# Performance work log

Hardware: AMD Instinct MI355X
Metric: run time of the kernel (lower is better)

The kernel has to match this reference:

```python
import jax, jax.numpy as jnp
import numpy as np


def _binarize(w):
    # BinaryConnect-style deterministic binarization: sign with 0 -> +1.
    # Straight-through estimator: identity gradient.
    b = jnp.where(w >= 0, 1.0, -1.0).astype(w.dtype)
    return w + jax.lax.stop_gradient(b - w)


def setup_inputs() -> dict:
    key = jax.random.key(0)
    ks = jax.random.split(key, 9)
    B = 65536
    x = jax.random.normal(ks[0], (B, 784), dtype=jnp.float32)
    # Kaiming-ish latent fp32 weights for the binary layers, fp32 final layer.
    w1 = jax.random.normal(ks[1], (512, 784), dtype=jnp.float32) * (1.0 / np.sqrt(784))
    b1 = jnp.zeros((512,), dtype=jnp.float32)
    w2 = jax.random.normal(ks[2], (512, 512), dtype=jnp.float32) * (1.0 / np.sqrt(512))
    b2 = jnp.zeros((512,), dtype=jnp.float32)
    w3 = jax.random.normal(ks[3], (512, 512), dtype=jnp.float32) * (1.0 / np.sqrt(512))
    b3 = jnp.zeros((512,), dtype=jnp.float32)
    w4 = jax.random.normal(ks[4], (10, 512), dtype=jnp.float32) * (1.0 / np.sqrt(512))
    b4 = jnp.zeros((10,), dtype=jnp.float32)
    return {"x": x, "w1": w1, "b1": b1, "w2": w2, "b2": b2,
            "w3": w3, "b3": b3, "w4": w4, "b4": b4}


def reference(x, w1, b1, w2, b2, w3, b3, w4, b4):
    # fc1..fc3: binarized-weight linear + ReLU; fc4: plain fp32 linear.
    h = jax.nn.relu(x @ _binarize(w1).T + b1)
    h = jax.nn.relu(h @ _binarize(w2).T + b2)
    h = jax.nn.relu(h @ _binarize(w3).T + b3)
    return h @ w4.T + b4
```

## Files before the change

kernel.cpp:

```cpp
#include <hip/hip_runtime.h>
#include <hip/hip_bf16.h>
#include <stdint.h>


typedef __attribute__((ext_vector_type(8))) short short8;
typedef __attribute__((ext_vector_type(4))) float f32x4;

#define THREADS 512
#define BM      64
#define HID     512
#define K1      784
#define K1P     832
#define BK      32
#define NK1     (K1P / BK)
#define NK2     (HID / BK)

#define M1_OFF  0
#define M1_BYTES (8 * NK1 * 256)
#define M2_OFF  (M1_OFF + M1_BYTES)
#define M2_BYTES (8 * NK2 * 256)
#define M3_OFF  (M2_OFF + M2_BYTES)
#define W4_OFF  (M3_OFF + M2_BYTES)
#define W4_BYTES (16 * HID * 2)
#define WS_BYTES (W4_OFF + W4_BYTES)

#define H_BYTES  (BM * HID * 2)
#define XBUF0    H_BYTES
#define XTILE_SZ (BM * BK * 2)
#define LUT_OFF  (XBUF0 + 2 * XTILE_SZ)
#define LDS_TOTAL (LUT_OFF + 128)

#define LGKM0_BARRIER()  do {                                   \
    asm volatile("s_waitcnt lgkmcnt(0)" ::: "memory");          \
    __builtin_amdgcn_s_barrier();                               \
} while (0)

__device__ __forceinline__ unsigned short bfu(float f) {
    __hip_bfloat16 h = __float2bfloat16(f);
    return *reinterpret_cast<unsigned short*>(&h);
}

__device__ __forceinline__ unsigned cvtpk(float lo, float hi) {
    unsigned d;
    asm("v_cvt_pk_bf16_f32 %0, %1, %2" : "=v"(d) : "v"(lo), "v"(hi));
    return d;
}

__global__ void prep_weights(const float* __restrict__ w1, const float* __restrict__ w2,
                             const float* __restrict__ w3, const float* __restrict__ w4,
                             unsigned char* __restrict__ ws)
{
    int id = blockIdx.x * blockDim.x + threadIdx.x;
    const int T1 = 8 * NK1 * 64;
    const int T2 = 8 * NK2 * 64;
    const int T4 = 16 * (HID / 16);

    if (id < T1) {
        int wn = id / (NK1 * 64), rem = id % (NK1 * 64);
        int kt = rem / 64, lane = rem % 64;
        int lr = lane & 15, lg = lane >> 4;
        unsigned m = 0;
#pragma unroll
        for (int nf = 0; nf < 4; ++nf) {
            int n = wn * 64 + nf * 16 + lr;
#pragma unroll
            for (int j = 0; j < 8; ++j) {
                int k = kt * BK + lg * 8 + j;
                if (k < K1 && w1[n * K1 + k] < 0.0f) m |= 1u << (nf * 8 + j);
            }
        }
        *(unsigned*)(ws + M1_OFF + (size_t)id * 4) = m;
        return;
    }
    id -= T1;
    if (id < 2 * T2) {
        const float* w = (id < T2) ? w2 : w3;
        unsigned base = (id < T2) ? M2_OFF : M3_OFF;
        int iid = (id < T2) ? id : id - T2;
        int wn = iid / (NK2 * 64), rem = iid % (NK2 * 64);
        int kt = rem / 64, lane = rem % 64;
        int lr = lane & 15, lg = lane >> 4;
        unsigned m = 0;
#pragma unroll
        for (int nf = 0; nf < 4; ++nf) {
            int n = wn * 64 + nf * 16 + lr;
#pragma unroll
            for (int j = 0; j < 8; ++j) {
                int k = kt * BK + lg * 8 + j;
                if (w[n * HID + k] < 0.0f) m |= 1u << (nf * 8 + j);
            }
        }
        *(unsigned*)(ws + base + (size_t)iid * 4) = m;
        return;
    }
    id -= 2 * T2;
    if (id < T4) {
        int n = id / (HID / 16), j = id % (HID / 16);
        int kp0 = j * 16;
        unsigned short v[16];
#pragma unroll
        for (int i = 0; i < 16; ++i)
            v[i] = (n < 10) ? bfu(w4[n * HID + kp0 + i]) : 0;
        unsigned off = W4_OFF + n * 1024 + kp0 * 2;
        *(short8*)(ws + off)      = *(short8*)&v[0];
        *(short8*)(ws + off + 16) = *(short8*)&v[8];
    }
}

__global__ __launch_bounds__(THREADS, 4)
void fused_mlp(const float* __restrict__ x,
               const unsigned char* __restrict__ ws,
               const float* __restrict__ b1, const float* __restrict__ b2,
               const float* __restrict__ b3, const float* __restrict__ b4,
               float* __restrict__ out)
{
    extern __shared__ unsigned char lds[];
    const int tid  = threadIdx.x;
    const int lane = tid & 63;
    const int wave = tid >> 6;
    const int lr   = lane & 15;
    const int lg   = lane >> 4;
    const int row_base = blockIdx.x * BM;
    const unsigned swz = (unsigned)((lr & 7) << 4);

    if (tid < 16) {
        unsigned e0 = ((tid & 1) ? 0xBF80u : 0x3F80u)
                    | (((tid & 2) ? 0xBF80u : 0x3F80u) << 16);
        unsigned e1 = ((tid & 4) ? 0xBF80u : 0x3F80u)
                    | (((tid & 8) ? 0xBF80u : 0x3F80u) << 16);
        uint2 e; e.x = e0; e.y = e1;
        *(uint2*)(lds + LUT_OFF + tid * 8) = e;
    }

    f32x4 acc[4][4];
    auto zeroAcc = [&]() {
#pragma unroll
        for (int nf = 0; nf < 4; ++nf)
#pragma unroll
            for (int mg = 0; mg < 4; ++mg)
                acc[nf][mg] = (f32x4){0.f, 0.f, 0.f, 0.f};
    };

    auto h_off = [&](int row, int bc) -> unsigned {
        return ((unsigned)(row * 1024 + bc)) ^ (unsigned)((row & 7) << 4);
    };

    auto epilogueToH = [&](const float* __restrict__ bias) {
#pragma unroll
        for (int nf = 0; nf < 4; ++nf) {
            const int n0 = wave * 64 + nf * 16 + lg * 4;
            float4 bv = *(const float4*)(bias + n0);
#pragma unroll
            for (int mg = 0; mg < 4; ++mg) {
                float v0 = acc[nf][mg][0] + bv.x; v0 = v0 > 0.f ? v0 : 0.f;
                float v1 = acc[nf][mg][1] + bv.y; v1 = v1 > 0.f ? v1 : 0.f;
                float v2 = acc[nf][mg][2] + bv.z; v2 = v2 > 0.f ? v2 : 0.f;
                float v3 = acc[nf][mg][3] + bv.w; v3 = v3 > 0.f ? v3 : 0.f;
                uint2 d; d.x = cvtpk(v0, v1); d.y = cvtpk(v2, v3);
                int row = mg * 16 + lr;
                unsigned off = ((unsigned)(row * 1024 + n0 * 2)) ^ (unsigned)((row & 7) << 4);
                *(uint2*)(lds + off) = d;
            }
        }
    };

    auto lutA = [&](unsigned m, int nf) -> short8 {
        unsigned lo = (m >> (nf * 8)) & 15u;
        unsigned hi = (m >> (nf * 8 + 4)) & 15u;
        union { short8 s; uint2 d[2]; } r;
        r.d[0] = *(const uint2*)(lds + LUT_OFF + lo * 8);
        r.d[1] = *(const uint2*)(lds + LUT_OFF + hi * 8);
        return r.s;
    };

    {
        zeroAcc();
        const unsigned char* mb1 = ws + M1_OFF + wave * (NK1 * 256) + lane * 4;
        const int srow = tid >> 3, sq = tid & 7;
        const float* xrow = x + (size_t)(row_base + srow) * K1;
        const unsigned s_off = (((unsigned)(srow * 64 + sq * 8)) ^ (unsigned)((srow & 7) << 4)) + XBUF0;
        const unsigned xbase = (((unsigned)(lr * 64 + lg * 16)) ^ swz) + XBUF0;

        auto xload = [&](int t) -> float4 {
            int col = t * BK + sq * 4;
            return (col < K1) ? *(const float4*)(xrow + col)
                              : make_float4(0.f, 0.f, 0.f, 0.f);
        };
        auto stage_write = [&](int buf, float4 v) {
            uint2 pk; pk.x = cvtpk(v.x, v.y); pk.y = cvtpk(v.z, v.w);
            *(uint2*)(lds + s_off + buf * XTILE_SZ) = pk;
        };
        auto mload1 = [&](int t) -> unsigned {
            int tc = t < NK1 ? t : NK1 - 1;
            return *(const unsigned*)(mb1 + tc * 256);
        };
        auto l1_compute = [&](int buf, unsigned m) {
            unsigned xb = xbase + buf * XTILE_SZ;
            short8 B0 = *(const short8*)(lds + xb);
            short8 B1 = *(const short8*)(lds + xb + 1024);
            short8 B2 = *(const short8*)(lds + xb + 2048);
            short8 B3 = *(const short8*)(lds + xb + 3072);
            __builtin_amdgcn_s_setprio(1);
#pragma unroll
            for (int nf = 0; nf < 4; ++nf) {
                short8 A = lutA(m, nf);
                acc[nf][0] = __builtin_amdgcn_mfma_f32_16x16x32_bf16(A, B0, acc[nf][0], 0, 0, 0);
                acc[nf][1] = __builtin_amdgcn_mfma_f32_16x16x32_bf16(A, B1, acc[nf][1], 0, 0, 0);
                acc[nf][2] = __builtin_amdgcn_mfma_f32_16x16x32_bf16(A, B2, acc[nf][2], 0, 0, 0);
                acc[nf][3] = __builtin_amdgcn_mfma_f32_16x16x32_bf16(A, B3, acc[nf][3], 0, 0, 0);
            }
            __builtin_amdgcn_s_setprio(0);
        };

        stage_write(0, xload(0));
        float4 xc = xload(1), xn = xload(2);
        unsigned mc = mload1(0), mn = mload1(1);
        LGKM0_BARRIER();

#pragma unroll 1
        for (int kt = 0; kt < NK1; ++kt) {
            float4 xnew = xload(kt + 3);
            unsigned mnew = mload1(kt + 2);
            l1_compute(kt & 1, mc);
            stage_write((kt + 1) & 1, xc);
            xc = xn; xn = xnew; mc = mn; mn = mnew;
            LGKM0_BARRIER();
        }

        epilogueToH(b1);
        LGKM0_BARRIER();
    }

#pragma unroll 1
    for (int layer = 0; layer < 2; ++layer) {
        const unsigned char* mb = ws + (layer == 0 ? M2_OFF : M3_OFF)
                                + wave * (NK2 * 256) + lane * 4;
        const float* bias = (layer == 0) ? b2 : b3;

        zeroAcc();

        auto mload2 = [&](int t) -> unsigned {
            int tc = t < NK2 ? t : NK2 - 1;
            return *(const unsigned*)(mb + tc * 256);
        };
        auto l23_compute = [&](int kt, unsigned m) {
            unsigned hb = (((unsigned)(lr * 1024 + kt * 64 + lg * 16)) ^ swz);
            short8 B0 = *(const short8*)(lds + hb);
            short8 B1 = *(const short8*)(lds + hb + 16384);
            short8 B2 = *(const short8*)(lds + hb + 32768);
            short8 B3 = *(const short8*)(lds + hb + 49152);
            __builtin_amdgcn_s_setprio(1);
#pragma unroll
            for (int nf = 0; nf < 4; ++nf) {
                short8 A = lutA(m, nf);
                acc[nf][0] = __builtin_amdgcn_mfma_f32_16x16x32_bf16(A, B0, acc[nf][0], 0, 0, 0);
                acc[nf][1] = __builtin_amdgcn_mfma_f32_16x16x32_bf16(A, B1, acc[nf][1], 0, 0, 0);
                acc[nf][2] = __builtin_amdgcn_mfma_f32_16x16x32_bf16(A, B2, acc[nf][2], 0, 0, 0);
                acc[nf][3] = __builtin_amdgcn_mfma_f32_16x16x32_bf16(A, B3, acc[nf][3], 0, 0, 0);
            }
            __builtin_amdgcn_s_setprio(0);
        };

        unsigned q0 = mload2(0), q1 = mload2(1), q2 = mload2(2), q3 = mload2(3);
#pragma unroll 1
        for (int kt = 0; kt < NK2; kt += 4) {
            l23_compute(kt + 0, q0); q0 = mload2(kt + 4);
            l23_compute(kt + 1, q1); q1 = mload2(kt + 5);
            l23_compute(kt + 2, q2); q2 = mload2(kt + 6);
            l23_compute(kt + 3, q3); q3 = mload2(kt + 7);
        }

        LGKM0_BARRIER();
        epilogueToH(bias);
        LGKM0_BARRIER();
    }

    if (wave < 4) {
        const unsigned char* w4b = ws + W4_OFF + lr * 1024 + lg * 16;
        const int m = wave * 16 + lr;
        short8 w4f[16];
#pragma unroll
        for (int kt = 0; kt < NK2; ++kt)
            w4f[kt] = *(const short8*)(w4b + kt * 64);
        f32x4 acc4 = (f32x4){0.f, 0.f, 0.f, 0.f};
#pragma unroll
        for (int kt = 0; kt < NK2; ++kt) {
            short8 a = *(const short8*)(lds + h_off(m, kt * 64 + lg * 16));
            acc4 = __builtin_amdgcn_mfma_f32_16x16x32_bf16(a, w4f[kt], acc4, 0, 0, 0);
        }
        if (lr < 10) {
            float bv = b4[lr];
#pragma unroll
            for (int r = 0; r < 4; ++r) {
                int row = row_base + wave * 16 + lg * 4 + r;
                out[(size_t)row * 10 + lr] = acc4[r] + bv;
            }
        }
    }
}

extern "C" void kernel_launch(void* const* d_in, const int* in_sizes, int n_in,
                              void* d_out, int out_size, void* d_ws, size_t ws_size,
                              hipStream_t stream) {
    const float* x  = (const float*)d_in[0];
    const float* w1 = (const float*)d_in[1];
    const float* b1 = (const float*)d_in[2];
    const float* w2 = (const float*)d_in[3];
    const float* b2 = (const float*)d_in[4];
    const float* w3 = (const float*)d_in[5];
    const float* b3 = (const float*)d_in[6];
    const float* w4 = (const float*)d_in[7];
    const float* b4 = (const float*)d_in[8];
    float* out = (float*)d_out;
    unsigned char* ws = (unsigned char*)d_ws;

    if (ws_size < (size_t)WS_BYTES) return;

    const int B = in_sizes[0] / K1;
    const int nblk = B / BM;

    (void)hipFuncSetAttribute((const void*)fused_mlp,
                              hipFuncAttributeMaxDynamicSharedMemorySize, LDS_TOTAL);

    const int prep_total = 8 * NK1 * 64 + 2 * (8 * NK2 * 64) + 16 * (HID / 16);
    prep_weights<<<(prep_total + 255) / 256, 256, 0, stream>>>(w1, w2, w3, w4, ws);
    fused_mlp<<<nblk, THREADS, LDS_TOTAL, stream>>>(x, ws, b1, b2, b3, b4, out);
}
```

Measured before the change: 106.8 us.

## Switch binary-MLP GEMMs from 16x16x32 to 32x32x16 bf16 MFMA tiles

Replaces the 16 per-step 16x16x32 MFMAs with 8 32x32x16 MFMAs on four 32x32 accumulator tiles. The weight sign-mask packing and the activation LDS fragment addressing are rewritten to match the 32-lane operand layout. The sign LUT is replicated four times in LDS and indexed by lane&3 to spread bank accesses. The aim is fewer MFMA issues and fewer operand loads per K step, at the cost of a new fragment layout and a rewritten epilogue that must stay correct.

```diff
diff --git a/kernel.cpp b/kernel.cpp
--- a/kernel.cpp
+++ b/kernel.cpp
@@ -3,8 +3,9 @@
 #include <stdint.h>
 
 
-typedef __attribute__((ext_vector_type(8))) short short8;
-typedef __attribute__((ext_vector_type(4))) float f32x4;
+typedef __attribute__((ext_vector_type(8)))  short short8;
+typedef __attribute__((ext_vector_type(4)))  float f32x4;
+typedef __attribute__((ext_vector_type(16))) float f32x16;
 
 #define THREADS 512
 #define BM      64
@@ -28,7 +29,7 @@
 #define XBUF0    H_BYTES
 #define XTILE_SZ (BM * BK * 2)
 #define LUT_OFF  (XBUF0 + 2 * XTILE_SZ)
-#define LDS_TOTAL (LUT_OFF + 128)
+#define LDS_TOTAL (LUT_OFF + 512)
 
 #define LGKM0_BARRIER()  do {                                   \
     asm volatile("s_waitcnt lgkmcnt(0)" ::: "memory");          \
@@ -58,15 +59,16 @@
     if (id < T1) {
         int wn = id / (NK1 * 64), rem = id % (NK1 * 64);
         int kt = rem / 64, lane = rem % 64;
-        int lr = lane & 15, lg = lane >> 4;
+        int r32 = lane & 31, g32 = lane >> 5;
         unsigned m = 0;
 #pragma unroll
-        for (int nf = 0; nf < 4; ++nf) {
-            int n = wn * 64 + nf * 16 + lr;
+        for (int f = 0; f < 4; ++f) {
+            int n = wn * 64 + (f >> 1) * 32 + r32;
+            int kb = kt * BK + (f & 1) * 16 + g32 * 8;
 #pragma unroll
             for (int j = 0; j < 8; ++j) {
-                int k = kt * BK + lg * 8 + j;
-                if (k < K1 && w1[n * K1 + k] < 0.0f) m |= 1u << (nf * 8 + j);
+                int k = kb + j;
+                if (k < K1 && w1[n * K1 + k] < 0.0f) m |= 1u << (f * 8 + j);
             }
         }
         *(unsigned*)(ws + M1_OFF + (size_t)id * 4) = m;
@@ -79,16 +81,15 @@
         int iid = (id < T2) ? id : id - T2;
         int wn = iid / (NK2 * 64), rem = iid % (NK2 * 64);
         int kt = rem / 64, lane = rem % 64;
-        int lr = lane & 15, lg = lane >> 4;
+        int r32 = lane & 31, g32 = lane >> 5;
         unsigned m = 0;
 #pragma unroll
-        for (int nf = 0; nf < 4; ++nf) {
-            int n = wn * 64 + nf * 16 + lr;
-#pragma unroll
-            for (int j = 0; j < 8; ++j) {
-                int k = kt * BK + lg * 8 + j;
-                if (w[n * HID + k] < 0.0f) m |= 1u << (nf * 8 + j);
-            }
+        for (int f = 0; f < 4; ++f) {
+            int n = wn * 64 + (f >> 1) * 32 + r32;
+            int kb = kt * BK + (f & 1) * 16 + g32 * 8;
+#pragma unroll
+            for (int j = 0; j < 8; ++j)
+                if (w[n * HID + kb + j] < 0.0f) m |= 1u << (f * 8 + j);
         }
         *(unsigned*)(ws + base + (size_t)iid * 4) = m;
         return;
@@ -120,58 +121,64 @@
     const int wave = tid >> 6;
     const int lr   = lane & 15;
     const int lg   = lane >> 4;
+    const int l31  = lane & 31;
+    const int l5   = lane >> 5;
     const int row_base = blockIdx.x * BM;
-    const unsigned swz = (unsigned)((lr & 7) << 4);
-
-    if (tid < 16) {
-        unsigned e0 = ((tid & 1) ? 0xBF80u : 0x3F80u)
-                    | (((tid & 2) ? 0xBF80u : 0x3F80u) << 16);
-        unsigned e1 = ((tid & 4) ? 0xBF80u : 0x3F80u)
-                    | (((tid & 8) ? 0xBF80u : 0x3F80u) << 16);
+    const unsigned swz = (unsigned)((lane & 7) << 4);
+    const unsigned lutbase = LUT_OFF + (unsigned)((lane & 3) << 7);
+
+    if (tid < 64) {
+        int entry = tid & 15;
+        unsigned e0 = ((entry & 1) ? 0xBF80u : 0x3F80u)
+                    | (((entry & 2) ? 0xBF80u : 0x3F80u) << 16);
+        unsigned e1 = ((entry & 4) ? 0xBF80u : 0x3F80u)
+                    | (((entry & 8) ? 0xBF80u : 0x3F80u) << 16);
         uint2 e; e.x = e0; e.y = e1;
-        *(uint2*)(lds + LUT_OFF + tid * 8) = e;
-    }
-
-    f32x4 acc[4][4];
+        *(uint2*)(lds + LUT_OFF + (tid >> 4) * 128 + entry * 8) = e;
+    }
+
+    f32x16 acc00, acc01, acc10, acc11;
     auto zeroAcc = [&]() {
-#pragma unroll
-        for (int nf = 0; nf < 4; ++nf)
-#pragma unroll
-            for (int mg = 0; mg < 4; ++mg)
-                acc[nf][mg] = (f32x4){0.f, 0.f, 0.f, 0.f};
+        f32x16 z;
+#pragma unroll
+        for (int i = 0; i < 16; ++i) z[i] = 0.f;
+        acc00 = z; acc01 = z; acc10 = z; acc11 = z;
     };
 
     auto h_off = [&](int row, int bc) -> unsigned {
         return ((unsigned)(row * 1024 + bc)) ^ (unsigned)((row & 7) << 4);
     };
 
+    auto lutA = [&](unsigned m, int f) -> short8 {
+        unsigned lo = (m >> (f * 8)) & 15u;
+        unsigned hi = (m >> (f * 8 + 4)) & 15u;
+        union { short8 s; uint2 d[2]; } r;
+        r.d[0] = *(const uint2*)(lds + lutbase + lo * 8);
+        r.d[1] = *(const uint2*)(lds + lutbase + hi * 8);
+        return r.s;
+    };
+
+    auto epi = [&](const f32x16& a, int nt, int bt, const float* __restrict__ bias) {
+        const int brow = bt * 32 + l31;
+#pragma unroll
+        for (int q = 0; q < 4; ++q) {
+            int n0 = wave * 64 + nt * 32 + 8 * q + 4 * l5;
+            float4 bv = *(const float4*)(bias + n0);
+            float v0 = a[4 * q + 0] + bv.x; v0 = v0 > 0.f ? v0 : 0.f;
+            float v1 = a[4 * q + 1] + bv.y; v1 = v1 > 0.f ? v1 : 0.f;
+            float v2 = a[4 * q + 2] + bv.z; v2 = v2 > 0.f ? v2 : 0.f;
+            float v3 = a[4 * q + 3] + bv.w; v3 = v3 > 0.f ? v3 : 0.f;
+            uint2 d; d.x = cvtpk(v0, v1); d.y = cvtpk(v2, v3);
+            unsigned off = ((unsigned)(brow * 1024 + n0 * 2)) ^ (unsigned)((brow & 7) << 4);
+            *(uint2*)(lds + off) = d;
+        }
+    };
     auto epilogueToH = [&](const float* __restrict__ bias) {
-#pragma unroll
-        for (int nf = 0; nf < 4; ++nf) {
-            const int n0 = wave * 64 + nf * 16 + lg * 4;
-            float4 bv = *(const float4*)(bias + n0);
-#pragma unroll
-            for (int mg = 0; mg < 4; ++mg) {
-                float v0 = acc[nf][mg][0] + bv.x; v0 = v0 > 0.f ? v0 : 0.f;
-                float v1 = acc[nf][mg][1] + bv.y; v1 = v1 > 0.f ? v1 : 0.f;
-                float v2 = acc[nf][mg][2] + bv.z; v2 = v2 > 0.f ? v2 : 0.f;
-                float v3 = acc[nf][mg][3] + bv.w; v3 = v3 > 0.f ? v3 : 0.f;
-                uint2 d; d.x = cvtpk(v0, v1); d.y = cvtpk(v2, v3);
-                int row = mg * 16 + lr;
-                unsigned off = ((unsigned)(row * 1024 + n0 * 2)) ^ (unsigned)((row & 7) << 4);
-                *(uint2*)(lds + off) = d;
-            }
-        }
-    };
-
-    auto lutA = [&](unsigned m, int nf) -> short8 {
-        unsigned lo = (m >> (nf * 8)) & 15u;
-        unsigned hi = (m >> (nf * 8 + 4)) & 15u;
-        union { short8 s; uint2 d[2]; } r;
-        r.d[0] = *(const uint2*)(lds + LUT_OFF + lo * 8);
-        r.d[1] = *(const uint2*)(lds + LUT_OFF + hi * 8);
-        return r.s;
-    };
+        epi(acc00, 0, 0, bias); epi(acc01, 0, 1, bias);
+        epi(acc10, 1, 0, bias); epi(acc11, 1, 1, bias);
+    };
+
+#define MFMA32(A, B, C) C = __builtin_amdgcn_mfma_f32_32x32x16_bf16(A, B, C, 0, 0, 0)
 
     {
         zeroAcc();
@@ -179,7 +186,8 @@
         const int srow = tid >> 3, sq = tid & 7;
         const float* xrow = x + (size_t)(row_base + srow) * K1;
         const unsigned s_off = (((unsigned)(srow * 64 + sq * 8)) ^ (unsigned)((srow & 7) << 4)) + XBUF0;
-        const unsigned xbase = (((unsigned)(lr * 64 + lg * 16)) ^ swz) + XBUF0;
+        const unsigned x00 = (((unsigned)(l31 * 64 + l5 * 16)) ^ swz) + XBUF0;
+        const unsigned x01 = (((unsigned)(l31 * 64 + 32 + l5 * 16)) ^ swz) + XBUF0;
 
         auto xload = [&](int t) -> float4 {
             int col = t * BK + sq * 4;
@@ -195,20 +203,18 @@
             return *(const unsigned*)(mb1 + tc * 256);
         };
         auto l1_compute = [&](int buf, unsigned m) {
-            unsigned xb = xbase + buf * XTILE_SZ;
-            short8 B0 = *(const short8*)(lds + xb);
-            short8 B1 = *(const short8*)(lds + xb + 1024);
-            short8 B2 = *(const short8*)(lds + xb + 2048);
-            short8 B3 = *(const short8*)(lds + xb + 3072);
+            unsigned b0 = x00 + buf * XTILE_SZ, b1 = x01 + buf * XTILE_SZ;
+            short8 B00 = *(const short8*)(lds + b0);
+            short8 B01 = *(const short8*)(lds + b1);
+            short8 B10 = *(const short8*)(lds + b0 + 2048);
+            short8 B11 = *(const short8*)(lds + b1 + 2048);
+            short8 A00 = lutA(m, 0), A01 = lutA(m, 1);
+            short8 A10 = lutA(m, 2), A11 = lutA(m, 3);
             __builtin_amdgcn_s_setprio(1);
-#pragma unroll
-            for (int nf = 0; nf < 4; ++nf) {
-                short8 A = lutA(m, nf);
-                acc[nf][0] = __builtin_amdgcn_mfma_f32_16x16x32_bf16(A, B0, acc[nf][0], 0, 0, 0);
-                acc[nf][1] = __builtin_amdgcn_mfma_f32_16x16x32_bf16(A, B1, acc[nf][1], 0, 0, 0);
-                acc[nf][2] = __builtin_amdgcn_mfma_f32_16x16x32_bf16(A, B2, acc[nf][2], 0, 0, 0);
-                acc[nf][3] = __builtin_amdgcn_mfma_f32_16x16x32_bf16(A, B3, acc[nf][3], 0, 0, 0);
-            }
+            MFMA32(A00, B00, acc00); MFMA32(A01, B01, acc00);
+            MFMA32(A00, B10, acc01); MFMA32(A01, B11, acc01);
+            MFMA32(A10, B00, acc10); MFMA32(A11, B01, acc10);
+            MFMA32(A10, B10, acc11); MFMA32(A11, B11, acc11);
             __builtin_amdgcn_s_setprio(0);
         };
 
@@ -244,20 +250,19 @@
             return *(const unsigned*)(mb + tc * 256);
         };
         auto l23_compute = [&](int kt, unsigned m) {
-            unsigned hb = (((unsigned)(lr * 1024 + kt * 64 + lg * 16)) ^ swz);
-            short8 B0 = *(const short8*)(lds + hb);
-            short8 B1 = *(const short8*)(lds + hb + 16384);
-            short8 B2 = *(const short8*)(lds + hb + 32768);
-            short8 B3 = *(const short8*)(lds + hb + 49152);
+            unsigned h0 = (((unsigned)(l31 * 1024 + kt * 64 + l5 * 16)) ^ swz);
+            unsigned h1 = (((unsigned)(l31 * 1024 + kt * 64 + 32 + l5 * 16)) ^ swz);
+            short8 B00 = *(const short8*)(lds + h0);
+            short8 B01 = *(const short8*)(lds + h1);
+            short8 B10 = *(const short8*)(lds + h0 + 32768);
+            short8 B11 = *(const short8*)(lds + h1 + 32768);
+            short8 A00 = lutA(m, 0), A01 = lutA(m, 1);
+            short8 A10 = lutA(m, 2), A11 = lutA(m, 3);
             __builtin_amdgcn_s_setprio(1);
-#pragma unroll
-            for (int nf = 0; nf < 4; ++nf) {
-                short8 A = lutA(m, nf);
-                acc[nf][0] = __builtin_amdgcn_mfma_f32_16x16x32_bf16(A, B0, acc[nf][0], 0, 0, 0);
-                acc[nf][1] = __builtin_amdgcn_mfma_f32_16x16x32_bf16(A, B1, acc[nf][1], 0, 0, 0);
-                acc[nf][2] = __builtin_amdgcn_mfma_f32_16x16x32_bf16(A, B2, acc[nf][2], 0, 0, 0);
-                acc[nf][3] = __builtin_amdgcn_mfma_f32_16x16x32_bf16(A, B3, acc[nf][3], 0, 0, 0);
-            }
+            MFMA32(A00, B00, acc00); MFMA32(A01, B01, acc00);
+            MFMA32(A00, B10, acc01); MFMA32(A01, B11, acc01);
+            MFMA32(A10, B00, acc10); MFMA32(A11, B01, acc10);
+            MFMA32(A10, B10, acc11); MFMA32(A11, B11, acc11);
             __builtin_amdgcn_s_setprio(0);
         };
 
@@ -297,6 +302,7 @@
             }
         }
     }
+#undef MFMA32
 }
 
 extern "C" void kernel_launch(void* const* d_in, const int* in_sizes, int n_in,
```

After: 132.2 us. 23.8% more time.

## Double-buffer hidden LDS fragments, replicate sign LUT, trim layer-1 K padding

Applied to the files above, without the earlier changes.

Layers 2–3 now load the next k-step's four B fragments from LDS into a second register buffer while the current step's MFMAs run, so LDS reads overlap compute. The ±1 sign LUT is replicated four times and indexed by lane, which spreads LUT lookups across more LDS banks. Layer-1 K padding is reduced from 832 to 800, removing one 32-wide k-tile of zero work. The added register buffer raises VGPR pressure under the 4-blocks launch bound, and the shorter padding relies on the hidden layer-1 loop handling the new tile count.

```diff
diff --git a/kernel.cpp b/kernel.cpp
--- a/kernel.cpp
+++ b/kernel.cpp
@@ -10,7 +10,7 @@
 #define BM      64
 #define HID     512
 #define K1      784
-#define K1P     832
+#define K1P     800
 #define BK      32
 #define NK1     (K1P / BK)
 #define NK2     (HID / BK)
@@ -28,7 +28,7 @@
 #define XBUF0    H_BYTES
 #define XTILE_SZ (BM * BK * 2)
 #define LUT_OFF  (XBUF0 + 2 * XTILE_SZ)
-#define LDS_TOTAL (LUT_OFF + 128)
+#define LDS_TOTAL (LUT_OFF + 512)
 
 #define LGKM0_BARRIER()  do {                                   \
     asm volatile("s_waitcnt lgkmcnt(0)" ::: "memory");          \
@@ -122,14 +122,16 @@
     const int lg   = lane >> 4;
     const int row_base = blockIdx.x * BM;
     const unsigned swz = (unsigned)((lr & 7) << 4);
-
-    if (tid < 16) {
-        unsigned e0 = ((tid & 1) ? 0xBF80u : 0x3F80u)
-                    | (((tid & 2) ? 0xBF80u : 0x3F80u) << 16);
-        unsigned e1 = ((tid & 4) ? 0xBF80u : 0x3F80u)
-                    | (((tid & 8) ? 0xBF80u : 0x3F80u) << 16);
+    const unsigned lutbase = LUT_OFF + (unsigned)((lane & 3) << 7);
+
+    if (tid < 64) {
+        int entry = tid & 15;
+        unsigned e0 = ((entry & 1) ? 0xBF80u : 0x3F80u)
+                    | (((entry & 2) ? 0xBF80u : 0x3F80u) << 16);
+        unsigned e1 = ((entry & 4) ? 0xBF80u : 0x3F80u)
+                    | (((entry & 8) ? 0xBF80u : 0x3F80u) << 16);
         uint2 e; e.x = e0; e.y = e1;
-        *(uint2*)(lds + LUT_OFF + tid * 8) = e;
+        *(uint2*)(lds + LUT_OFF + (tid >> 4) * 128 + entry * 8) = e;
     }
 
     f32x4 acc[4][4];
@@ -168,8 +170,8 @@
         unsigned lo = (m >> (nf * 8)) & 15u;
         unsigned hi = (m >> (nf * 8 + 4)) & 15u;
         union { short8 s; uint2 d[2]; } r;
-        r.d[0] = *(const uint2*)(lds + LUT_OFF + lo * 8);
-        r.d[1] = *(const uint2*)(lds + LUT_OFF + hi * 8);
+        r.d[0] = *(const uint2*)(lds + lutbase + lo * 8);
+        r.d[1] = *(const uint2*)(lds + lutbase + hi * 8);
         return r.s;
     };
 
@@ -243,31 +245,36 @@
             int tc = t < NK2 ? t : NK2 - 1;
             return *(const unsigned*)(mb + tc * 256);
         };
-        auto l23_compute = [&](int kt, unsigned m) {
-            unsigned hb = (((unsigned)(lr * 1024 + kt * 64 + lg * 16)) ^ swz);
-            short8 B0 = *(const short8*)(lds + hb);
-            short8 B1 = *(const short8*)(lds + hb + 16384);
-            short8 B2 = *(const short8*)(lds + hb + 32768);
-            short8 B3 = *(const short8*)(lds + hb + 49152);
+        auto loadBH = [&](short8 (&B)[4], int t) {
+            int tc = t < NK2 ? t : NK2 - 1;
+            unsigned hb = (((unsigned)(lr * 1024 + tc * 64 + lg * 16)) ^ swz);
+            B[0] = *(const short8*)(lds + hb);
+            B[1] = *(const short8*)(lds + hb + 16384);
+            B[2] = *(const short8*)(lds + hb + 32768);
+            B[3] = *(const short8*)(lds + hb + 49152);
+        };
+        auto l23_compute = [&](short8 (&B)[4], unsigned m) {
             __builtin_amdgcn_s_setprio(1);
 #pragma unroll
             for (int nf = 0; nf < 4; ++nf) {
                 short8 A = lutA(m, nf);
-                acc[nf][0] = __builtin_amdgcn_mfma_f32_16x16x32_bf16(A, B0, acc[nf][0], 0, 0, 0);
-                acc[nf][1] = __builtin_amdgcn_mfma_f32_16x16x32_bf16(A, B1, acc[nf][1], 0, 0, 0);
-                acc[nf][2] = __builtin_amdgcn_mfma_f32_16x16x32_bf16(A, B2, acc[nf][2], 0, 0, 0);
-                acc[nf][3] = __builtin_amdgcn_mfma_f32_16x16x32_bf16(A, B3, acc[nf][3], 0, 0, 0);
+                acc[nf][0] = __builtin_amdgcn_mfma_f32_16x16x32_bf16(A, B[0], acc[nf][0], 0, 0, 0);
+                acc[nf][1] = __builtin_amdgcn_mfma_f32_16x16x32_bf16(A, B[1], acc[nf][1], 0, 0, 0);
+                acc[nf][2] = __builtin_amdgcn_mfma_f32_16x16x32_bf16(A, B[2], acc[nf][2], 0, 0, 0);
+                acc[nf][3] = __builtin_amdgcn_mfma_f32_16x16x32_bf16(A, B[3], acc[nf][3], 0, 0, 0);
             }
             __builtin_amdgcn_s_setprio(0);
         };
 
         unsigned q0 = mload2(0), q1 = mload2(1), q2 = mload2(2), q3 = mload2(3);
+        short8 Ba[4], Bb[4];
+        loadBH(Ba, 0);
 #pragma unroll 1
         for (int kt = 0; kt < NK2; kt += 4) {
-            l23_compute(kt + 0, q0); q0 = mload2(kt + 4);
-            l23_compute(kt + 1, q1); q1 = mload2(kt + 5);
-            l23_compute(kt + 2, q2); q2 = mload2(kt + 6);
-            l23_compute(kt + 3, q3); q3 = mload2(kt + 7);
+            loadBH(Bb, kt + 1); l23_compute(Ba, q0); q0 = mload2(kt + 4);
+            loadBH(Ba, kt + 2); l23_compute(Bb, q1); q1 = mload2(kt + 5);
+            loadBH(Bb, kt + 3); l23_compute(Ba, q2); q2 = mload2(kt + 6);
+            loadBH(Ba, kt + 4); l23_compute(Bb, q3); q3 = mload2(kt + 7);
         }
 
         LGKM0_BARRIER();
```

Result: slower. 159.2 us (+49.1%).
